# Optimization experiments

Hardware: AMD Instinct MI355X
Metric: run time of the kernel (lower is better)

The kernel has to match this reference:

```python
import jax, jax.numpy as jnp
import numpy as np

CHANNELS = 256
C_QK = CHANNELS // 8


def setup_inputs() -> dict:
    key = jax.random.key(0)
    ks = jax.random.split(key, 7)
    b, c, h, w = 8, CHANNELS, 64, 64
    x = jax.random.normal(ks[0], (b, c, h, w), dtype=jnp.float32)
    # 1x1 conv weights stored as [out_ch, in_ch]; biases [out_ch]
    s = 1.0 / np.sqrt(c)
    wq = jax.random.uniform(ks[1], (C_QK, c), jnp.float32, -s, s)
    bq = jax.random.uniform(ks[2], (C_QK,), jnp.float32, -s, s)
    wk = jax.random.uniform(ks[3], (C_QK, c), jnp.float32, -s, s)
    bk = jax.random.uniform(ks[4], (C_QK,), jnp.float32, -s, s)
    wv = jax.random.uniform(ks[5], (c, c), jnp.float32, -s, s)
    bv = jax.random.uniform(ks[6], (c,), jnp.float32, -s, s)
    return {"x": x, "wq": wq, "bq": bq, "wk": wk, "bk": bk, "wv": wv, "bv": bv}


def reference(x, wq, bq, wk, bk, wv, bv):
    b, c, h, w = x.shape
    xf = x.reshape(b, c, h * w)  # [b, c, n]
    # 1x1 convs == per-pixel linear projections
    q = jnp.einsum('oc,bcn->bon', wq, xf) + bq[None, :, None]  # [b, c//8, n]
    k = jnp.einsum('oc,bcn->bon', wk, xf) + bk[None, :, None]  # [b, c//8, n]
    v = jnp.einsum('oc,bcn->bon', wv, xf) + bv[None, :, None]  # [b, c, n]
    # attention[i, j] = q_i . k_j  (no scaling, matching the torch code)
    attn = jnp.einsum('bdi,bdj->bij', q, k)  # [b, n, n]
    attn = jax.nn.softmax(attn, axis=-1)
    # out[:, :, i] = sum_j attn[i, j] * v[:, :, j]
    out = jnp.einsum('bij,bcj->bci', attn, v)  # [b, c, n]
    return out.reshape(b, c, h, w)
```

## Files before the change

### kernel.cpp

```cpp
#include <hip/hip_runtime.h>
#include <stdint.h>

#define NB 8
#define NC 256
#define ND 32
#define NN 4096
#define QT 64
#define KT 32
#define NBUF 3

typedef __attribute__((ext_vector_type(8))) short short8;
typedef __attribute__((ext_vector_type(4))) float float4_;

#define MFMA16(a,b,c) __builtin_amdgcn_mfma_f32_16x16x32_bf16((a),(b),(c),0,0,0)

#if __has_builtin(__builtin_amdgcn_exp2f)
#define EXP2(x) __builtin_amdgcn_exp2f(x)
#else
#define EXP2(x) exp2f(x)
#endif
#define L2E 1.44269504088896f
#define SCB (24.0f * L2E)

__device__ __forceinline__ uint16_t f2bf(float f) {
  uint32_t u = __builtin_bit_cast(uint32_t, f);
  u += 0x7fffu + ((u >> 16) & 1u);
  return (uint16_t)(u >> 16);
}
__device__ __forceinline__ float bf2f(uint16_t h) {
  uint32_t u = (uint32_t)h << 16;
  return __builtin_bit_cast(float, u);
}
__device__ __forceinline__ short8 ld8(const uint16_t* p) {
  return *reinterpret_cast<const short8*>(p);
}
__device__ __forceinline__ void async16(const uint16_t* g, uint16_t* l) {
  __builtin_amdgcn_global_load_lds(
      (const __attribute__((address_space(1))) uint32_t*)g,
      (__attribute__((address_space(3))) uint32_t*)l, 16, 0, 0);
}
__device__ __forceinline__ void fbar() {
  asm volatile("" ::: "memory");
  __builtin_amdgcn_s_barrier();
  asm volatile("" ::: "memory");
}

__global__ __launch_bounds__(256) void k_prep(
    const float* __restrict__ x, const float* __restrict__ wq,
    const float* __restrict__ wk, const float* __restrict__ wv,
    uint16_t* __restrict__ xTh, uint16_t* __restrict__ xTl,
    uint16_t* __restrict__ Wh, uint16_t* __restrict__ Wl, int use_xl)
{
  int bx = blockIdx.x, tid = threadIdx.x;
  if (bx >= 2048) {
    int e = (bx - 2048) * 256 + tid;
    int r = e >> 8;
    float w = (r < 32) ? wq[e] : (r < 64) ? wk[e - 32 * 256] : wv[e - 64 * 256];
    uint16_t h = f2bf(w);
    Wh[e] = h;
    Wl[e] = f2bf(w - bf2f(h));
    return;
  }
  __shared__ uint32_t tile[64][65];
  int b = bx >> 8, t = bx & 255;
  int c0 = (t >> 6) << 6, n0 = (t & 63) << 6;
  const float* xb = x + ((size_t)b * NC + c0) * NN + n0;
  int cc = tid >> 4, nw = (tid & 15) << 2;
  for (int i = 0; i < 4; i++) {
    int c = cc + 16 * i;
    float4_ v = *reinterpret_cast<const float4_*>(xb + (size_t)c * NN + nw);
    for (int u = 0; u < 4; u++) {
      uint16_t h = f2bf(v[u]);
      uint16_t l = f2bf(v[u] - bf2f(h));
      tile[c][nw + u] = (uint32_t)h | ((uint32_t)l << 16);
    }
  }
  __syncthreads();
  int cw = (tid & 15) << 2, nn = tid >> 4;
  for (int i = 0; i < 4; i++) {
    int n = nn + 16 * i;
    uint32_t p0 = tile[cw + 0][n], p1 = tile[cw + 1][n];
    uint32_t p2 = tile[cw + 2][n], p3 = tile[cw + 3][n];
    size_t o = ((size_t)b * NN + n0 + n) * NC + c0 + cw;
    *(uint32_t*)(xTh + o)     = (p0 & 0xffffu) | (p1 << 16);
    *(uint32_t*)(xTh + o + 2) = (p2 & 0xffffu) | (p3 << 16);
    if (use_xl) {
      *(uint32_t*)(xTl + o)     = (p0 >> 16) | (p1 & 0xffff0000u);
      *(uint32_t*)(xTl + o + 2) = (p2 >> 16) | (p3 & 0xffff0000u);
    }
  }
}

__global__ __launch_bounds__(256) void k_qkv(
    const uint16_t* __restrict__ xTh, const uint16_t* __restrict__ xTl,
    const uint16_t* __restrict__ Wh, const uint16_t* __restrict__ Wl,
    const float* __restrict__ bq, const float* __restrict__ bk,
    const float* __restrict__ bv,
    uint16_t* __restrict__ Qh, uint16_t* __restrict__ Ql,
    uint16_t* __restrict__ Kh, uint16_t* __restrict__ Kl,
    uint16_t* __restrict__ V, int use_xl, int use_lo)
{
  int b = blockIdx.x & 7, n0 = (blockIdx.x >> 3) * 64;
  int tid = threadIdx.x, wid = tid >> 6, lane = tid & 63;
  int l15 = lane & 15, quad = lane >> 4;
  int nb = n0 + wid * 16;
  float4_ acc[20];
  for (int m = 0; m < 20; m++) acc[m] = (float4_){0.f, 0.f, 0.f, 0.f};
  for (int ks = 0; ks < 8; ks++) {
    size_t xa = ((size_t)b * NN + nb + l15) * NC + ks * 32 + quad * 8;
    short8 bh = ld8(xTh + xa);
    short8 blo;
    if (use_xl) blo = ld8(xTl + xa);
    for (int mt = 0; mt < 20; mt++) {
      size_t wa = (size_t)(16 * mt + l15) * NC + ks * 32 + quad * 8;
      short8 ah = ld8(Wh + wa);
      acc[mt] = MFMA16(ah, bh, acc[mt]);
      if (mt < 4) {
        short8 al = ld8(Wl + wa);
        acc[mt] = MFMA16(al, bh, acc[mt]);
      }
      if (use_xl) acc[mt] = MFMA16(ah, blo, acc[mt]);
    }
  }
  int n = nb + l15;
  for (int mt = 0; mt < 20; mt++) {
    for (int r = 0; r < 4; r++) {
      int row = 16 * mt + quad * 4 + r;
      float v = acc[mt][r];
      if (mt < 2) {
        v = (v + bq[row]) * L2E;
        size_t o = ((size_t)b * NN + n) * ND + row;
        uint16_t h = f2bf(v);
        Qh[o] = h;
        if (use_lo) Ql[o] = f2bf(v - bf2f(h));
      } else if (mt < 4) {
        int rk = row - 32;
        v += bk[rk];
        size_t o = ((size_t)b * NN + n) * ND + rk;
        uint16_t h = f2bf(v);
        Kh[o] = h;
        if (use_lo) Kl[o] = f2bf(v - bf2f(h));
      } else {
        int c = row - 64;
        v += bv[c];
        V[((size_t)b * NC + c) * NN + n] = f2bf(v);
      }
    }
  }
}

__global__ __launch_bounds__(512) void k_attn(
    const uint16_t* __restrict__ Qh, const uint16_t* __restrict__ Ql,
    const uint16_t* __restrict__ Kh, const uint16_t* __restrict__ Kl,
    const uint16_t* __restrict__ V, float* __restrict__ out, int use_lo)
{
  __shared__ uint16_t sV[NBUF][256][KT];
  __shared__ uint16_t sP[4][16][40];
  __shared__ float sL[QT];

  int bx = blockIdx.x;
  int b = bx & 7;
  int q0 = (bx >> 3) * QT;
  int tid = threadIdx.x, wid = tid >> 6, lane = tid & 63;
  int l15 = lane & 15, quad = lane >> 4;
  const size_t qkb = (size_t)b * NN * ND;
  const uint16_t* Vb = V + (size_t)b * NC * NN;
  const bool heavy = (wid < 4);

  int sw = (l15 >> 1) & 3;
  auto stageV = [&](int j) {
    int buf = j % NBUF;
    int j0 = j * KT;
    for (int i = 0; i < 4; i++) {
      int sl = (wid - 4) * 256 + 64 * i + lane;
      int c = sl >> 2;
      int q2s = (sl & 3) ^ ((sl >> 3) & 3);
      const uint16_t* g = Vb + (size_t)c * NN + j0 + q2s * 8;
      uint16_t* l = &sV[buf][0][0] + ((wid - 4) * 4 + i) * 512;
      async16(g, l);
    }
  };

  float4_ acc[2][4];
  for (int m = 0; m < 2; m++) for (int n = 0; n < 4; n++)
    acc[m][n] = (float4_){0.f, 0.f, 0.f, 0.f};
  float l_part = 0.f;

  short8 qfh, qfl, kh0, kh1, kl0, kl1;
  if (heavy) {
    size_t a = qkb + (size_t)(q0 + wid * 16 + l15) * ND + quad * 8;
    qfh = ld8(Qh + a);
    if (use_lo) qfl = ld8(Ql + a);
    size_t a0 = qkb + (size_t)l15 * ND + quad * 8;
    size_t a1 = qkb + (size_t)(16 + l15) * ND + quad * 8;
    kh0 = ld8(Kh + a0); kh1 = ld8(Kh + a1);
    if (use_lo) { kl0 = ld8(Kl + a0); kl1 = ld8(Kl + a1); }
  } else {
    stageV(0);
    stageV(1);
  }

  for (int j = 0; j < NN / KT; j++) {
    int buf = j % NBUF;
    if (heavy) {
      short8 nh0, nh1, nl0, nl1;
      if (j < NN / KT - 1) {
        size_t a0 = qkb + (size_t)((j + 1) * KT + l15) * ND + quad * 8;
        size_t a1 = a0 + 16 * ND;
        nh0 = ld8(Kh + a0); nh1 = ld8(Kh + a1);
        if (use_lo) { nl0 = ld8(Kl + a0); nl1 = ld8(Kl + a1); }
      }
      float4_ S0 = (float4_){0.f,0.f,0.f,0.f}, S1 = S0;
      S0 = MFMA16(kh0, qfh, S0);
      S1 = MFMA16(kh1, qfh, S1);
      if (use_lo) {
        S0 = MFMA16(kl0, qfh, S0); S0 = MFMA16(kh0, qfl, S0);
        S1 = MFMA16(kl1, qfh, S1); S1 = MFMA16(kh1, qfl, S1);
      }
      float p0[4], p1[4];
      for (int r = 0; r < 4; r++) {
        p0[r] = EXP2(S0[r] - SCB);
        p1[r] = EXP2(S1[r] - SCB);
      }
      l_part += ((p0[0] + p0[1]) + (p0[2] + p0[3])) +
                ((p1[0] + p1[1]) + (p1[2] + p1[3]));
      uint2 w0, w1;
      w0.x = (uint32_t)f2bf(p0[0]) | ((uint32_t)f2bf(p0[1]) << 16);
      w0.y = (uint32_t)f2bf(p0[2]) | ((uint32_t)f2bf(p0[3]) << 16);
      w1.x = (uint32_t)f2bf(p1[0]) | ((uint32_t)f2bf(p1[1]) << 16);
      w1.y = (uint32_t)f2bf(p1[2]) | ((uint32_t)f2bf(p1[3]) << 16);
      *reinterpret_cast<uint2*>(&sP[wid][l15][4 * quad]) = w0;
      *reinterpret_cast<uint2*>(&sP[wid][l15][16 + 4 * quad]) = w1;
      kh0 = nh0; kh1 = nh1;
      if (use_lo) { kl0 = nl0; kl1 = nl1; }
      asm volatile("s_waitcnt lgkmcnt(0)" ::: "memory");
    } else {
      if (j < NN / KT - 2) {
        stageV(j + 2);
        asm volatile("s_waitcnt vmcnt(8)" ::: "memory");
      } else {
        asm volatile("s_waitcnt vmcnt(0)" ::: "memory");
      }
    }
    fbar();
    short8 bfP[4];
    for (int qt = 0; qt < 4; qt++)
      bfP[qt] = ld8(&sP[qt][l15][quad * 8]);
    for (int mt = 0; mt < 2; mt++) {
      short8 af = ld8(&sV[buf][wid * 32 + 16 * mt + l15][(quad ^ sw) * 8]);
      for (int qt = 0; qt < 4; qt++)
        acc[mt][qt] = MFMA16(af, bfP[qt], acc[mt][qt]);
    }
    asm volatile("s_waitcnt lgkmcnt(0)" ::: "memory");
    fbar();
  }

  if (heavy) {
    float l_tot = l_part;
    l_tot += __shfl_xor(l_tot, 16);
    l_tot += __shfl_xor(l_tot, 32);
    if (quad == 0) sL[wid * 16 + l15] = l_tot;
  }
  __syncthreads();
  float linv[4];
  for (int qt = 0; qt < 4; qt++) linv[qt] = 1.0f / sL[qt * 16 + l15];
  for (int mt = 0; mt < 2; mt++)
    for (int qt = 0; qt < 4; qt++)
      for (int r = 0; r < 4; r++) {
        int c = wid * 32 + 16 * mt + quad * 4 + r;
        int q = q0 + qt * 16 + l15;
        out[((size_t)(b * NC + c)) * NN + q] = acc[mt][qt][r] * linv[qt];
      }
}

extern "C" void kernel_launch(void* const* d_in, const int* in_sizes, int n_in,
                              void* d_out, int out_size, void* d_ws, size_t ws_size,
                              hipStream_t stream)
{
  const float* x  = (const float*)d_in[0];
  const float* wq = (const float*)d_in[1];
  const float* bq = (const float*)d_in[2];
  const float* wk = (const float*)d_in[3];
  const float* bk = (const float*)d_in[4];
  const float* wv = (const float*)d_in[5];
  const float* bv = (const float*)d_in[6];
  float* out = (float*)d_out;

  const size_t szXT = (size_t)NB * NN * NC * 2;
  const size_t szW  = (size_t)320 * 256 * 2;
  const size_t szQK = (size_t)NB * NN * ND * 2;
  const size_t szV  = (size_t)NB * NC * NN * 2;
  size_t needA = 2 * szXT + 2 * szW + 4 * szQK + szV;
  size_t needB = szXT + 2 * szW + 4 * szQK + szV;
  int use_xl = ws_size >= needA;
  int use_lo = ws_size >= needB;

  char* p = (char*)d_ws;
  uint16_t* xTh = (uint16_t*)p; p += szXT;
  uint16_t* xTl = use_xl ? (uint16_t*)p : xTh; if (use_xl) p += szXT;
  uint16_t* Wh = (uint16_t*)p; p += szW;
  uint16_t* Wl = (uint16_t*)p; p += szW;
  uint16_t* Qh = (uint16_t*)p; p += szQK;
  uint16_t* Ql = use_lo ? (uint16_t*)p : xTh; if (use_lo) p += szQK;
  uint16_t* Kh = (uint16_t*)p; p += szQK;
  uint16_t* Kl = use_lo ? (uint16_t*)p : xTh; if (use_lo) p += szQK;
  uint16_t* Vw = (uint16_t*)p;

  hipLaunchKernelGGL(k_prep, dim3(2368), dim3(256), 0, stream,
                     x, wq, wk, wv, xTh, xTl, Wh, Wl, use_xl);
  hipLaunchKernelGGL(k_qkv, dim3(512), dim3(256), 0, stream,
                     xTh, xTl, Wh, Wl, bq, bk, bv, Qh, Ql, Kh, Kl, Vw,
                     use_xl, use_lo);
  hipLaunchKernelGGL(k_attn, dim3(512), dim3(512), 0, stream,
                     Qh, Ql, Kh, Kl, Vw, out, use_lo);
}
```

Measured before the change: 286.0 us.

## Software-pipeline attention loop with double-buffered P and 4-stage V ring

New measurement: 277.7 us. 2.9% less time.

```diff
diff --git a/kernel.cpp b/kernel.cpp
--- a/kernel.cpp
+++ b/kernel.cpp
@@ -7,7 +7,7 @@
 #define NN 4096
 #define QT 64
 #define KT 32
-#define NBUF 3
+#define NBUF 4
 
 typedef __attribute__((ext_vector_type(8))) short short8;
 typedef __attribute__((ext_vector_type(4))) float float4_;
@@ -33,6 +33,11 @@
 }
 __device__ __forceinline__ short8 ld8(const uint16_t* p) {
   return *reinterpret_cast<const short8*>(p);
+}
+__device__ __forceinline__ uint32_t cvtpk(float lo, float hi) {
+  uint32_t r;
+  asm("v_cvt_pk_bf16_f32 %0, %1, %2" : "=v"(r) : "v"(lo), "v"(hi));
+  return r;
 }
 __device__ __forceinline__ void async16(const uint16_t* g, uint16_t* l) {
   __builtin_amdgcn_global_load_lds(
@@ -149,13 +154,13 @@
   }
 }
 
-__global__ __launch_bounds__(512) void k_attn(
+__global__ __launch_bounds__(512, 4) void k_attn(
     const uint16_t* __restrict__ Qh, const uint16_t* __restrict__ Ql,
     const uint16_t* __restrict__ Kh, const uint16_t* __restrict__ Kl,
     const uint16_t* __restrict__ V, float* __restrict__ out, int use_lo)
 {
   __shared__ uint16_t sV[NBUF][256][KT];
-  __shared__ uint16_t sP[4][16][40];
+  __shared__ uint16_t sP[2][4][16][40];
   __shared__ float sL[QT];
 
   int bx = blockIdx.x;
@@ -168,17 +173,27 @@
   const bool heavy = (wid < 4);
 
   int sw = (l15 >> 1) & 3;
-  auto stageV = [&](int j) {
-    int buf = j % NBUF;
-    int j0 = j * KT;
-    for (int i = 0; i < 4; i++) {
-      int sl = (wid - 4) * 256 + 64 * i + lane;
-      int c = sl >> 2;
-      int q2s = (sl & 3) ^ ((sl >> 3) & 3);
-      const uint16_t* g = Vb + (size_t)c * NN + j0 + q2s * 8;
-      uint16_t* l = &sV[buf][0][0] + ((wid - 4) * 4 + i) * 512;
-      async16(g, l);
-    }
+
+  const uint16_t* gp0; const uint16_t* gp1;
+  const uint16_t* gp2; const uint16_t* gp3;
+  uint32_t off0, off1, off2, off3;
+  if (!heavy) {
+#define INITGP(i, GP, OFF)                                   \
+    { int sl = (wid - 4) * 256 + 64 * i + lane;              \
+      int c = sl >> 2;                                       \
+      int q2s = (sl & 3) ^ ((sl >> 3) & 3);                  \
+      GP = Vb + (size_t)c * NN + q2s * 8;                    \
+      OFF = (uint32_t)(((wid - 4) * 4 + i) * 512); }
+    INITGP(0, gp0, off0) INITGP(1, gp1, off1)
+    INITGP(2, gp2, off2) INITGP(3, gp3, off3)
+#undef INITGP
+  }
+  auto stage = [&](int s) {
+    uint16_t* base = &sV[0][0][0] + (size_t)(s & 3) * 8192;
+    async16(gp0, base + off0); gp0 += KT;
+    async16(gp1, base + off1); gp1 += KT;
+    async16(gp2, base + off2); gp2 += KT;
+    async16(gp3, base + off3); gp3 += KT;
   };
 
   float4_ acc[2][4];
@@ -187,69 +202,82 @@
   float l_part = 0.f;
 
   short8 qfh, qfl, kh0, kh1, kl0, kl1;
+  const uint16_t* pKh = Kh + qkb + (size_t)l15 * ND + quad * 8;
+  const uint16_t* pKl = Kl + qkb + (size_t)l15 * ND + quad * 8;
+
+  auto qkt = [&](int sb, short8 h0, short8 h1, short8 lo0, short8 lo1) {
+    float4_ S0 = (float4_){0.f, 0.f, 0.f, 0.f}, S1 = S0;
+    S0 = MFMA16(h0, qfh, S0);
+    S1 = MFMA16(h1, qfh, S1);
+    if (use_lo) {
+      S0 = MFMA16(lo0, qfh, S0); S0 = MFMA16(h0, qfl, S0);
+      S1 = MFMA16(lo1, qfh, S1); S1 = MFMA16(h1, qfl, S1);
+    }
+    float p0[4], p1[4];
+#pragma unroll
+    for (int r = 0; r < 4; r++) {
+      p0[r] = EXP2(S0[r] - SCB);
+      p1[r] = EXP2(S1[r] - SCB);
+    }
+    l_part += ((p0[0] + p0[1]) + (p0[2] + p0[3])) +
+              ((p1[0] + p1[1]) + (p1[2] + p1[3]));
+    uint2 w0, w1;
+    w0.x = cvtpk(p0[0], p0[1]); w0.y = cvtpk(p0[2], p0[3]);
+    w1.x = cvtpk(p1[0], p1[1]); w1.y = cvtpk(p1[2], p1[3]);
+    *reinterpret_cast<uint2*>(&sP[sb][wid][l15][4 * quad]) = w0;
+    *reinterpret_cast<uint2*>(&sP[sb][wid][l15][16 + 4 * quad]) = w1;
+  };
+
   if (heavy) {
     size_t a = qkb + (size_t)(q0 + wid * 16 + l15) * ND + quad * 8;
     qfh = ld8(Qh + a);
     if (use_lo) qfl = ld8(Ql + a);
-    size_t a0 = qkb + (size_t)l15 * ND + quad * 8;
-    size_t a1 = qkb + (size_t)(16 + l15) * ND + quad * 8;
-    kh0 = ld8(Kh + a0); kh1 = ld8(Kh + a1);
-    if (use_lo) { kl0 = ld8(Kl + a0); kl1 = ld8(Kl + a1); }
+    short8 t0 = ld8(pKh), t1 = ld8(pKh + 512), tl0, tl1;
+    if (use_lo) { tl0 = ld8(pKl); tl1 = ld8(pKl + 512); }
+    qkt(0, t0, t1, tl0, tl1);
+    kh0 = ld8(pKh + 1024); kh1 = ld8(pKh + 1536);
+    if (use_lo) { kl0 = ld8(pKl + 1024); kl1 = ld8(pKl + 1536); }
+    pKh += 2048; pKl += 2048;
+    asm volatile("s_waitcnt lgkmcnt(0)" ::: "memory");
   } else {
-    stageV(0);
-    stageV(1);
-  }
+    stage(0); stage(1); stage(2);
+    asm volatile("s_waitcnt vmcnt(8)" ::: "memory");
+  }
+  fbar();
 
   for (int j = 0; j < NN / KT; j++) {
-    int buf = j % NBUF;
+    int buf = j & 3;
+    int pb = j & 1;
     if (heavy) {
       short8 nh0, nh1, nl0, nl1;
-      if (j < NN / KT - 1) {
-        size_t a0 = qkb + (size_t)((j + 1) * KT + l15) * ND + quad * 8;
-        size_t a1 = a0 + 16 * ND;
-        nh0 = ld8(Kh + a0); nh1 = ld8(Kh + a1);
-        if (use_lo) { nl0 = ld8(Kl + a0); nl1 = ld8(Kl + a1); }
+      if (j < NN / KT - 2) {
+        nh0 = ld8(pKh); nh1 = ld8(pKh + 512);
+        if (use_lo) { nl0 = ld8(pKl); nl1 = ld8(pKl + 512); }
+        pKh += 1024; pKl += 1024;
       }
-      float4_ S0 = (float4_){0.f,0.f,0.f,0.f}, S1 = S0;
-      S0 = MFMA16(kh0, qfh, S0);
-      S1 = MFMA16(kh1, qfh, S1);
-      if (use_lo) {
-        S0 = MFMA16(kl0, qfh, S0); S0 = MFMA16(kh0, qfl, S0);
-        S1 = MFMA16(kl1, qfh, S1); S1 = MFMA16(kh1, qfl, S1);
-      }
-      float p0[4], p1[4];
-      for (int r = 0; r < 4; r++) {
-        p0[r] = EXP2(S0[r] - SCB);
-        p1[r] = EXP2(S1[r] - SCB);
-      }
-      l_part += ((p0[0] + p0[1]) + (p0[2] + p0[3])) +
-                ((p1[0] + p1[1]) + (p1[2] + p1[3]));
-      uint2 w0, w1;
-      w0.x = (uint32_t)f2bf(p0[0]) | ((uint32_t)f2bf(p0[1]) << 16);
-      w0.y = (uint32_t)f2bf(p0[2]) | ((uint32_t)f2bf(p0[3]) << 16);
-      w1.x = (uint32_t)f2bf(p1[0]) | ((uint32_t)f2bf(p1[1]) << 16);
-      w1.y = (uint32_t)f2bf(p1[2]) | ((uint32_t)f2bf(p1[3]) << 16);
-      *reinterpret_cast<uint2*>(&sP[wid][l15][4 * quad]) = w0;
-      *reinterpret_cast<uint2*>(&sP[wid][l15][16 + 4 * quad]) = w1;
+      if (j < NN / KT - 1)
+        qkt(pb ^ 1, kh0, kh1, kl0, kl1);
       kh0 = nh0; kh1 = nh1;
       if (use_lo) { kl0 = nl0; kl1 = nl1; }
-      asm volatile("s_waitcnt lgkmcnt(0)" ::: "memory");
     } else {
-      if (j < NN / KT - 2) {
-        stageV(j + 2);
-        asm volatile("s_waitcnt vmcnt(8)" ::: "memory");
-      } else {
-        asm volatile("s_waitcnt vmcnt(0)" ::: "memory");
-      }
-    }
-    fbar();
+      if (j < NN / KT - 3) stage(j + 3);
+    }
     short8 bfP[4];
+#pragma unroll
     for (int qt = 0; qt < 4; qt++)
-      bfP[qt] = ld8(&sP[qt][l15][quad * 8]);
+      bfP[qt] = ld8(&sP[pb][qt][l15][quad * 8]);
+#pragma unroll
     for (int mt = 0; mt < 2; mt++) {
       short8 af = ld8(&sV[buf][wid * 32 + 16 * mt + l15][(quad ^ sw) * 8]);
+#pragma unroll
       for (int qt = 0; qt < 4; qt++)
         acc[mt][qt] = MFMA16(af, bfP[qt], acc[mt][qt]);
+    }
+    if (!heavy) {
+      if (j < NN / KT - 3)
+        asm volatile("s_waitcnt vmcnt(8)" ::: "memory");
+      else
+        asm volatile("s_waitcnt vmcnt(0)" ::: "memory");
     }
     asm volatile("s_waitcnt lgkmcnt(0)" ::: "memory");
     fbar();
```
